# Kernel optimization log

Hardware: AMD Instinct MI355X
Metric: run time of the kernel (lower is better)

Reference implementation:

```python
import jax, jax.numpy as jnp
import numpy as np

B, S, D = 4, 4096, 768

def setup_inputs() -> dict:
    key = jax.random.key(0)
    kx, kq, kk, kv = jax.random.split(key, 4)
    x = jax.random.normal(kx, (B, S, D), dtype=jnp.float32)
    Wq = jax.random.normal(kq, (D, D), dtype=jnp.float32) * (D ** -0.5)
    Wk = jax.random.normal(kk, (D, D), dtype=jnp.float32) * (D ** -0.5)
    Wv = jax.random.normal(kv, (D, D), dtype=jnp.float32) * (D ** -0.5)
    return {"x": x, "Wq": Wq, "Wk": Wk, "Wv": Wv}

def reference(x, Wq, Wk, Wv):
    # q,k,v: [B,S,D]  (Linear with no bias)
    q = x @ Wq
    k = x @ Wk
    v = x @ Wv
    # full N x N causal score matrix, as in the original module
    scores = jnp.einsum('bqd,bkd->bqk', q, k)  # [B,S,S]
    seq = scores.shape[1]
    causal_mask = jnp.triu(jnp.ones((seq, seq), dtype=bool), k=1)  # True above diagonal
    scores = jnp.where(causal_mask[None, :, :], -jnp.inf, scores)
    scale = jnp.asarray(k.shape[-1], scores.dtype) ** 0.5
    weights = jax.nn.softmax(scores / scale, axis=-1)  # [B,S,S]
    # dropout p=0.0 -> identity (deterministic reference)
    context = jnp.einsum('bqk,bkd->bqd', weights, v)  # [B,S,D]
    return context
```

## Files before the change

kernel.cpp:

```cpp
#include <hip/hip_runtime.h>
#include <hip/hip_bf16.h>

typedef __attribute__((ext_vector_type(8))) _Float16 half8_t;
typedef __attribute__((ext_vector_type(4))) _Float16 half4_t;
typedef __attribute__((ext_vector_type(4))) float float4_t;

#define D_DIM 768
#define S_DIM 4096
#define B_DIM 4
#define M_DIM (B_DIM * S_DIM)
#define SD ((size_t)S_DIM * D_DIM)

#define GLOAD_LDS16(g, s)                                      \
  __builtin_amdgcn_global_load_lds(                            \
      (const __attribute__((address_space(1))) void*)(g),      \
      (__attribute__((address_space(3))) void*)(s), 16, 0, 0)

__device__ __forceinline__ float4_t mfma16(half8_t a, half8_t b, float4_t c) {
  return __builtin_amdgcn_mfma_f32_16x16x32_f16(a, b, c, 0, 0, 0);
}

__global__ __launch_bounds__(256) void cvt_x_kernel(const float* __restrict__ in,
                                                    _Float16* __restrict__ out, int n) {
  int i = (blockIdx.x * 256 + threadIdx.x) * 4;
  if (i < n) {
    float4 v = *(const float4*)(in + i);
    half4_t o;
    o.x = (_Float16)v.x; o.y = (_Float16)v.y; o.z = (_Float16)v.z; o.w = (_Float16)v.w;
    *(half4_t*)(out + i) = o;
  }
}

__global__ __launch_bounds__(256) void transpose_w_kernel(const float* __restrict__ W0,
                                                          const float* __restrict__ W1,
                                                          const float* __restrict__ W2,
                                                          _Float16* __restrict__ WT) {
  const float* W = (blockIdx.z == 0) ? W0 : (blockIdx.z == 1) ? W1 : W2;
  _Float16* o = WT + (size_t)blockIdx.z * D_DIM * D_DIM;
  __shared__ _Float16 tile[64][68];
  int k0 = blockIdx.x * 64, n0 = blockIdx.y * 64;
#pragma unroll
  for (int i = 0; i < 16; ++i) {
    int idx = threadIdx.x + i * 256;
    int r = idx >> 6, c = idx & 63;
    tile[r][c] = (_Float16)W[(size_t)(k0 + r) * D_DIM + n0 + c];
  }
  __syncthreads();
#pragma unroll
  for (int i = 0; i < 16; ++i) {
    int idx = threadIdx.x + i * 256;
    int r = idx >> 6, c = idx & 63;
    o[(size_t)(n0 + r) * D_DIM + k0 + c] = tile[c][r];
  }
}

template <bool SWAP>
__device__ __forceinline__ void core256(const _Float16* __restrict__ Ag,
                                        const _Float16* __restrict__ Bg,
                                        int lda, int ldb, int k0, int nt,
                                        char* lds, float4_t (&acc)[8][4]) {
  const int tid = threadIdx.x;
  const int w = tid >> 6, l = tid & 63;
  const int wr = w >> 2, wc = w & 3;
  const int l15 = l & 15, l4 = l >> 4;

  int aSrc[2], bSrc[2], sDst[2];
#pragma unroll
  for (int i = 0; i < 2; ++i) {
    int L = i * 512 + tid;
    int row = L >> 2, u = L & 3;
    int usw = u ^ ((row >> 1) & 3);
    aSrc[i] = row * lda + usw * 8;
    bSrc[i] = row * ldb + usw * 8;
    sDst[i] = (i * 512 + (tid & ~63)) * 16;
  }

#define STG(kt)                                                               \
  do {                                                                        \
    char* slot = lds + ((kt) & 3) * 32768;                                    \
    const _Float16* Asrc = Ag + (size_t)(k0 + (kt)) * 32;                     \
    const _Float16* Bsrc = Bg + (size_t)(k0 + (kt)) * 32;                     \
    _Pragma("unroll") for (int i = 0; i < 2; ++i)                             \
        GLOAD_LDS16(Asrc + aSrc[i], slot + sDst[i]);                          \
    _Pragma("unroll") for (int i = 0; i < 2; ++i)                             \
        GLOAD_LDS16(Bsrc + bSrc[i], slot + 16384 + sDst[i]);                  \
  } while (0)

#pragma unroll
  for (int j = 0; j < 3; ++j)
    if (j < nt) STG(j);

#pragma unroll 1
  for (int kt = 0; kt < nt; ++kt) {
    __builtin_amdgcn_s_barrier();
    if (kt + 3 < nt) STG(kt + 3);
    __builtin_amdgcn_sched_barrier(0);
    if (kt + 3 < nt)
      asm volatile("s_waitcnt vmcnt(12)" ::: "memory");
    else if (kt + 2 < nt)
      asm volatile("s_waitcnt vmcnt(8)" ::: "memory");
    else if (kt + 1 < nt)
      asm volatile("s_waitcnt vmcnt(4)" ::: "memory");
    else
      asm volatile("s_waitcnt vmcnt(0)" ::: "memory");
    __builtin_amdgcn_sched_barrier(0);
    __builtin_amdgcn_s_barrier();
    __builtin_amdgcn_sched_barrier(0);

    const char* As = lds + (kt & 3) * 32768;
    const char* Bs = As + 16384;
    half8_t bf[4];
#pragma unroll
    for (int ni = 0; ni < 4; ++ni) {
      int brow = wc * 64 + ni * 16 + l15;
      bf[ni] = *(const half8_t*)(Bs + brow * 64 + ((l4 ^ ((brow >> 1) & 3)) * 16));
    }
    __builtin_amdgcn_s_setprio(1);
#pragma unroll
    for (int mq = 0; mq < 2; ++mq) {
      half8_t af[4];
#pragma unroll
      for (int mi = 0; mi < 4; ++mi) {
        int arow = wr * 128 + (mq * 4 + mi) * 16 + l15;
        af[mi] = *(const half8_t*)(As + arow * 64 + ((l4 ^ ((arow >> 1) & 3)) * 16));
      }
#pragma unroll
      for (int mi = 0; mi < 4; ++mi)
#pragma unroll
        for (int ni = 0; ni < 4; ++ni) {
          if (SWAP)
            acc[mq * 4 + mi][ni] = mfma16(bf[ni], af[mi], acc[mq * 4 + mi][ni]);
          else
            acc[mq * 4 + mi][ni] = mfma16(af[mi], bf[ni], acc[mq * 4 + mi][ni]);
        }
    }
    __builtin_amdgcn_s_setprio(0);
  }
#undef STG
}

__global__ __launch_bounds__(512, 1) void proj8_kernel(const _Float16* __restrict__ xh,
                                                       const _Float16* __restrict__ WT,
                                                       _Float16* __restrict__ qkv,
                                                       _Float16* __restrict__ vt) {
  __shared__ __align__(16) char lds[131072];
  const int bid = blockIdx.x;
  const int wid = (bid & 7) * 72 + (bid >> 3);
  const int rg2 = wid / 18;
  const int rem = wid % 18;
  const int z = rem / 6;
  const int cb = (rem % 6) >> 1;
  const int rbg = rg2 * 2 + (rem & 1);

  const _Float16* Ag = xh + (size_t)rbg * 256 * D_DIM;
  const _Float16* Bg = WT + (size_t)z * D_DIM * D_DIM + (size_t)cb * 256 * D_DIM;
  float4_t acc[8][4];
#pragma unroll
  for (int a = 0; a < 8; ++a)
#pragma unroll
    for (int b = 0; b < 4; ++b) acc[a][b] = (float4_t){0.f, 0.f, 0.f, 0.f};

  const int tid = threadIdx.x;
  const int w = tid >> 6, l = tid & 63;
  const int wr = w >> 2, wc = w & 3;
  const int l15 = l & 15, l4 = l >> 4;

  if (z < 2) {
    core256<false>(Ag, Bg, D_DIM, D_DIM, 0, 24, lds, acc);
    _Float16* C = qkv + (size_t)z * M_DIM * D_DIM;
#pragma unroll
    for (int mi = 0; mi < 8; ++mi)
#pragma unroll
      for (int ni = 0; ni < 4; ++ni) {
        int col = cb * 256 + wc * 64 + ni * 16 + l15;
#pragma unroll
        for (int j = 0; j < 4; ++j) {
          int row = rbg * 256 + wr * 128 + mi * 16 + l4 * 4 + j;
          C[(size_t)row * D_DIM + col] = (_Float16)acc[mi][ni][j];
        }
      }
  } else {
    core256<true>(Ag, Bg, D_DIM, D_DIM, 0, 24, lds, acc);
#pragma unroll
    for (int mi = 0; mi < 8; ++mi) {
      int scol = rbg * 256 + wr * 128 + mi * 16 + l15;
      int bb = scol >> 12;
      int sl = scol & 4095;
      _Float16* vtb = vt + (size_t)bb * SD;
#pragma unroll
      for (int ni = 0; ni < 4; ++ni) {
#pragma unroll
        for (int j = 0; j < 4; ++j) {
          int drow = cb * 256 + wc * 64 + ni * 16 + l4 * 4 + j;
          vtb[(size_t)drow * S_DIM + sl] = (_Float16)acc[mi][ni][j];
        }
      }
    }
  }
}

__global__ __launch_bounds__(512, 1) void gemm1_8_kernel(const _Float16* __restrict__ Q,
                                                         const _Float16* __restrict__ K,
                                                         _Float16* __restrict__ P,
                                                         float* __restrict__ rp) {
  __shared__ __align__(16) char lds[131072];
  const float SCALE = 0.036084391824351615f;
  const int bid = blockIdx.x;
  const int wid = (bid & 7) * 68 + (bid >> 3);
  const int z = wid / 136;
  const int t = wid % 136;
  int g, base;
  if (t < 10) { g = 0; base = 0; }
  else if (t < 36) { g = 1; base = 10; }
  else if (t < 78) { g = 2; base = 36; }
  else { g = 3; base = 78; }
  int r = t - base;
  int rbg, cb;
  if (r < 16 * g) {
    int cbg = r >> 4, wi = r & 15;
    rbg = 4 * g + (wi >> 2);
    cb = 4 * cbg + (wi & 3);
  } else {
    int r2 = r - 16 * g;
    const int ri[10] = {0, 1, 1, 2, 2, 2, 3, 3, 3, 3};
    const int rj[10] = {0, 0, 1, 0, 1, 2, 0, 1, 2, 3};
    rbg = 4 * g + ri[r2];
    cb = 4 * g + rj[r2];
  }

  const _Float16* Ag = Q + (size_t)z * SD + (size_t)rbg * 256 * D_DIM;
  const _Float16* Bg = K + (size_t)z * SD + (size_t)cb * 256 * D_DIM;
  float4_t acc[8][4];
#pragma unroll
  for (int a = 0; a < 8; ++a)
#pragma unroll
    for (int b = 0; b < 4; ++b) acc[a][b] = (float4_t){0.f, 0.f, 0.f, 0.f};
  core256<false>(Ag, Bg, D_DIM, D_DIM, 0, 24, lds, acc);

  const int tid = threadIdx.x;
  const int w = tid >> 6, l = tid & 63;
  const int wr = w >> 2, wc = w & 3;
  const int l15 = l & 15, l4 = l >> 4;
  _Float16* Pz = P + (size_t)z * S_DIM * S_DIM;
  float* rpz = rp + (size_t)z * S_DIM * 64;
#pragma unroll
  for (int mi = 0; mi < 8; ++mi) {
#pragma unroll
    for (int j = 0; j < 4; ++j) {
      int row = rbg * 256 + wr * 128 + mi * 16 + l4 * 4 + j;
      float rs = 0.f;
#pragma unroll
      for (int ni = 0; ni < 4; ++ni) {
        int col = cb * 256 + wc * 64 + ni * 16 + l15;
        float v = (col <= row) ? __expf(acc[mi][ni][j] * SCALE - 4.0f) : 0.f;
        _Float16 ph = (_Float16)v;
        Pz[(size_t)row * S_DIM + col] = ph;
        rs += (float)ph;
      }
#pragma unroll
      for (int d = 1; d < 16; d <<= 1) rs += __shfl_xor(rs, d);
      if (l15 == 0) rpz[(size_t)row * 64 + cb * 4 + wc] = rs;
    }
  }
}

__global__ __launch_bounds__(256) void rsum_combine_kernel(const float* __restrict__ rp,
                                                           float* __restrict__ rsum) {
  int idx = blockIdx.x * 256 + threadIdx.x;
  int row = idx & 4095;
  int np = ((row >> 8) + 1) * 4;
  const float* p = rp + (size_t)idx * 64;
  float s = 0.f;
  for (int i = 0; i < np; ++i) s += p[i];
  rsum[idx] = s;
}

#define PART_STRIDE ((size_t)4 * 2048 * 768)
__global__ __launch_bounds__(512, 1) void gemm2_8_kernel(const _Float16* __restrict__ P,
                                                         const _Float16* __restrict__ VT,
                                                         float* __restrict__ outp,
                                                         _Float16* __restrict__ part,
                                                         const float* __restrict__ rsum) {
  __shared__ __align__(16) char lds[131072];
  const int bid = blockIdx.x;
  const int wid = (bid & 7) * 26 + (bid >> 3);
  if (wid >= 204) return;
  const int z = wid / 51;
  const int rem = wid % 51;
  const int u = rem / 3;
  const int by = rem % 3;
  int r1, c1, r2 = -1, c2 = 0;
  if (u < 9)        { r1 = 15 - u; c1 = 0; }
  else if (u == 9)  { r1 = 15;     c1 = 1; }
  else if (u < 13)  { r1 = 16 - u; c1 = 0; r2 = u - 10; c2 = 0; }
  else if (u == 13) { r1 = 3;      c1 = 0; r2 = 11;     c2 = 1; }
  else              { r1 = 28 - u; c1 = 1; r2 = u - 6;  c2 = 1; }

  const int tid = threadIdx.x;
  const int w = tid >> 6, l = tid & 63;
  const int wr = w >> 2, wc = w & 3;
  const int l15 = l & 15, l4 = l >> 4;
  const _Float16* Bg = VT + (size_t)z * SD + (size_t)by * 256 * S_DIM;

#pragma unroll 1
  for (int jj = 0; jj < 2; ++jj) {
    const int rbg = jj ? r2 : r1;
    if (rbg < 0) break;
    const int chk = jj ? c2 : c1;
    const int tot = 8 * (rbg + 1);
    const int k0 = chk * 64;
    const int nt = chk ? (tot - 64) : (tot < 64 ? tot : 64);
    const bool split = (tot > 64);
    if (jj) __syncthreads();

    const _Float16* Ag = P + (size_t)z * S_DIM * S_DIM + (size_t)rbg * 256 * S_DIM;
    float4_t acc[8][4];
#pragma unroll
    for (int a = 0; a < 8; ++a)
#pragma unroll
      for (int b = 0; b < 4; ++b) acc[a][b] = (float4_t){0.f, 0.f, 0.f, 0.f};
    core256<false>(Ag, Bg, S_DIM, S_DIM, k0, nt, lds, acc);

#pragma unroll
    for (int mi = 0; mi < 8; ++mi) {
#pragma unroll
      for (int j = 0; j < 4; ++j) {
        int row = rbg * 256 + wr * 128 + mi * 16 + l4 * 4 + j;
        if (!split) {
          float rinv = 1.0f / rsum[(size_t)z * S_DIM + row];
#pragma unroll
          for (int ni = 0; ni < 4; ++ni) {
            int col = by * 256 + wc * 64 + ni * 16 + l15;
            outp[(size_t)z * SD + (size_t)row * D_DIM + col] = acc[mi][ni][j] * rinv;
          }
        } else {
          int lr = row - 2048;
#pragma unroll
          for (int ni = 0; ni < 4; ++ni) {
            int col = by * 256 + wc * 64 + ni * 16 + l15;
            part[(size_t)chk * PART_STRIDE + ((size_t)z * 2048 + lr) * D_DIM + col] =
                (_Float16)acc[mi][ni][j];
          }
        }
      }
    }
  }
}

__global__ __launch_bounds__(256) void g2_combine_kernel(const _Float16* __restrict__ part,
                                                         const float* __restrict__ rsum,
                                                         float* __restrict__ outp) {
  int idx = blockIdx.x * 256 + threadIdx.x;
  int z = idx / 196608;
  int rem = idx - z * 196608;
  int lr = rem / 96, c8 = rem - lr * 96;
  size_t off = ((size_t)z * 2048 + lr) * D_DIM + c8 * 8;
  half8_t p0 = *(const half8_t*)(part + off);
  half8_t p1 = *(const half8_t*)(part + PART_STRIDE + off);
  int row = 2048 + lr;
  float rinv = 1.0f / rsum[(size_t)z * S_DIM + row];
  float* o = outp + (size_t)z * SD + (size_t)row * D_DIM + c8 * 8;
#pragma unroll
  for (int e = 0; e < 8; ++e) o[e] = ((float)p0[e] + (float)p1[e]) * rinv;
}

extern "C" void kernel_launch(void* const* d_in, const int* in_sizes, int n_in,
                              void* d_out, int out_size, void* d_ws, size_t ws_size,
                              hipStream_t stream) {
  const float* x = (const float*)d_in[0];
  const float* Wq = (const float*)d_in[1];
  const float* Wk = (const float*)d_in[2];
  const float* Wv = (const float*)d_in[3];
  float* out = (float*)d_out;
  char* ws = (char*)d_ws;

  const size_t XH_B = (size_t)M_DIM * D_DIM * 2;
  const size_t QKV_B = 3 * XH_B;
  const size_t VT_B = XH_B;
  const size_t WT_B = (size_t)3 * D_DIM * D_DIM * 2;
  const size_t BASE_END = XH_B + QKV_B + VT_B + WT_B;

  _Float16* xh = (_Float16*)ws;
  _Float16* qkv = (_Float16*)(ws + XH_B);
  _Float16* Q = qkv;
  _Float16* K = qkv + (size_t)M_DIM * D_DIM;
  _Float16* vt = (_Float16*)(ws + XH_B + QKV_B);
  _Float16* wt = (_Float16*)(ws + XH_B + QKV_B + VT_B);

  float* rp = (float*)(ws + BASE_END);
  float* rsum = (float*)(ws + BASE_END + (size_t)4194304);
  _Float16* P = (_Float16*)(ws + BASE_END + (size_t)4259840);
  _Float16* part = xh;

  cvt_x_kernel<<<dim3(12288), dim3(256), 0, stream>>>(x, xh, M_DIM * D_DIM);
  transpose_w_kernel<<<dim3(12, 12, 3), dim3(256), 0, stream>>>(Wq, Wk, Wv, wt);
  proj8_kernel<<<dim3(576), dim3(512), 0, stream>>>(xh, wt, qkv, vt);
  gemm1_8_kernel<<<dim3(544), dim3(512), 0, stream>>>(Q, K, P, rp);
  rsum_combine_kernel<<<dim3(64), dim3(256), 0, stream>>>(rp, rsum);
  gemm2_8_kernel<<<dim3(208), dim3(512), 0, stream>>>(P, vt, out, part, rsum);
  g2_combine_kernel<<<dim3(3072), dim3(256), 0, stream>>>(part, rsum, out);
}
```

Measured before the change: 299.7 us.

## Prefetch next k-tile LDS fragments into ping-pong registers in GEMM core

The shared GEMM core now loads the next k-tile's B and first-half A fragments from LDS while the current tile's MFMAs run. It alternates two register sets and unrolls the k-loop by two, and the vmcnt waits are shifted so each stage waits for tile kt+1 instead of kt. The goal is to hide LDS read latency behind matrix-core work. Separately, launch bounds on the three GEMM kernels change from one to two blocks per CU. Each block still uses 128 KB of LDS, so two blocks probably cannot share a CU, and the tighter register budget risks spilling the 128-float accumulator plus the extra fragment registers.

```diff
diff --git a/kernel.cpp b/kernel.cpp
--- a/kernel.cpp
+++ b/kernel.cpp
@@ -73,6 +73,20 @@
     aSrc[i] = row * lda + usw * 8;
     bSrc[i] = row * ldb + usw * 8;
     sDst[i] = (i * 512 + (tid & ~63)) * 16;
+  }
+
+  int bOff[4], a0Off[4], a1Off[4];
+#pragma unroll
+  for (int ni = 0; ni < 4; ++ni) {
+    int brow = wc * 64 + ni * 16 + l15;
+    bOff[ni] = 16384 + brow * 64 + ((l4 ^ ((brow >> 1) & 3)) * 16);
+  }
+#pragma unroll
+  for (int mi = 0; mi < 4; ++mi) {
+    int r0 = wr * 128 + mi * 16 + l15;
+    a0Off[mi] = r0 * 64 + ((l4 ^ ((r0 >> 1) & 3)) * 16);
+    int r1 = wr * 128 + (4 + mi) * 16 + l15;
+    a1Off[mi] = r1 * 64 + ((l4 ^ ((r1 >> 1) & 3)) * 16);
   }
 
 #define STG(kt)                                                               \
@@ -86,60 +100,76 @@
         GLOAD_LDS16(Bsrc + bSrc[i], slot + 16384 + sDst[i]);                  \
   } while (0)
 
-#pragma unroll
-  for (int j = 0; j < 3; ++j)
-    if (j < nt) STG(j);
-
-#pragma unroll 1
-  for (int kt = 0; kt < nt; ++kt) {
+  STG(0);
+  if (nt > 1) STG(1);
+  if (nt > 2) STG(2);
+  if (nt > 2)
+    asm volatile("s_waitcnt vmcnt(4)" ::: "memory");
+  else
+    asm volatile("s_waitcnt vmcnt(0)" ::: "memory");
+  __builtin_amdgcn_s_barrier();
+
+  half8_t bfA[4], a0A[4], bfB[4], a0B[4];
+#pragma unroll
+  for (int i = 0; i < 4; ++i) bfA[i] = *(const half8_t*)(lds + bOff[i]);
+#pragma unroll
+  for (int i = 0; i < 4; ++i) a0A[i] = *(const half8_t*)(lds + a0Off[i]);
+
+  auto phase = [&](int kt, half8_t (&bfC)[4], half8_t (&a0C)[4],
+                   half8_t (&bfN)[4], half8_t (&a0N)[4]) {
     __builtin_amdgcn_s_barrier();
     if (kt + 3 < nt) STG(kt + 3);
     __builtin_amdgcn_sched_barrier(0);
     if (kt + 3 < nt)
-      asm volatile("s_waitcnt vmcnt(12)" ::: "memory");
+      asm volatile("s_waitcnt vmcnt(8)" ::: "memory");
     else if (kt + 2 < nt)
-      asm volatile("s_waitcnt vmcnt(8)" ::: "memory");
-    else if (kt + 1 < nt)
       asm volatile("s_waitcnt vmcnt(4)" ::: "memory");
     else
       asm volatile("s_waitcnt vmcnt(0)" ::: "memory");
     __builtin_amdgcn_sched_barrier(0);
     __builtin_amdgcn_s_barrier();
-    __builtin_amdgcn_sched_barrier(0);
-
-    const char* As = lds + (kt & 3) * 32768;
-    const char* Bs = As + 16384;
-    half8_t bf[4];
-#pragma unroll
-    for (int ni = 0; ni < 4; ++ni) {
-      int brow = wc * 64 + ni * 16 + l15;
-      bf[ni] = *(const half8_t*)(Bs + brow * 64 + ((l4 ^ ((brow >> 1) & 3)) * 16));
+    const char* Sc = lds + (kt & 3) * 32768;
+    half8_t a1[4];
+#pragma unroll
+    for (int i = 0; i < 4; ++i) a1[i] = *(const half8_t*)(Sc + a1Off[i]);
+    if (kt + 1 < nt) {
+      const char* Sn = lds + ((kt + 1) & 3) * 32768;
+#pragma unroll
+      for (int i = 0; i < 4; ++i) bfN[i] = *(const half8_t*)(Sn + bOff[i]);
+#pragma unroll
+      for (int i = 0; i < 4; ++i) a0N[i] = *(const half8_t*)(Sn + a0Off[i]);
     }
     __builtin_amdgcn_s_setprio(1);
 #pragma unroll
-    for (int mq = 0; mq < 2; ++mq) {
-      half8_t af[4];
-#pragma unroll
-      for (int mi = 0; mi < 4; ++mi) {
-        int arow = wr * 128 + (mq * 4 + mi) * 16 + l15;
-        af[mi] = *(const half8_t*)(As + arow * 64 + ((l4 ^ ((arow >> 1) & 3)) * 16));
-      }
-#pragma unroll
-      for (int mi = 0; mi < 4; ++mi)
-#pragma unroll
-        for (int ni = 0; ni < 4; ++ni) {
-          if (SWAP)
-            acc[mq * 4 + mi][ni] = mfma16(bf[ni], af[mi], acc[mq * 4 + mi][ni]);
-          else
-            acc[mq * 4 + mi][ni] = mfma16(af[mi], bf[ni], acc[mq * 4 + mi][ni]);
-        }
-    }
+    for (int mi = 0; mi < 4; ++mi)
+#pragma unroll
+      for (int ni = 0; ni < 4; ++ni) {
+        if (SWAP)
+          acc[mi][ni] = mfma16(bfC[ni], a0C[mi], acc[mi][ni]);
+        else
+          acc[mi][ni] = mfma16(a0C[mi], bfC[ni], acc[mi][ni]);
+      }
+#pragma unroll
+    for (int mi = 0; mi < 4; ++mi)
+#pragma unroll
+      for (int ni = 0; ni < 4; ++ni) {
+        if (SWAP)
+          acc[4 + mi][ni] = mfma16(bfC[ni], a1[mi], acc[4 + mi][ni]);
+        else
+          acc[4 + mi][ni] = mfma16(a1[mi], bfC[ni], acc[4 + mi][ni]);
+      }
     __builtin_amdgcn_s_setprio(0);
+  };
+
+#pragma unroll 1
+  for (int kt = 0; kt < nt; kt += 2) {
+    phase(kt, bfA, a0A, bfB, a0B);
+    phase(kt + 1, bfB, a0B, bfA, a0A);
   }
 #undef STG
 }
 
-__global__ __launch_bounds__(512, 1) void proj8_kernel(const _Float16* __restrict__ xh,
+__global__ __launch_bounds__(512, 2) void proj8_kernel(const _Float16* __restrict__ xh,
                                                        const _Float16* __restrict__ WT,
                                                        _Float16* __restrict__ qkv,
                                                        _Float16* __restrict__ vt) {
@@ -199,7 +229,7 @@
   }
 }
 
-__global__ __launch_bounds__(512, 1) void gemm1_8_kernel(const _Float16* __restrict__ Q,
+__global__ __launch_bounds__(512, 2) void gemm1_8_kernel(const _Float16* __restrict__ Q,
                                                          const _Float16* __restrict__ K,
                                                          _Float16* __restrict__ P,
                                                          float* __restrict__ rp) {
@@ -276,7 +306,7 @@
 }
 
 #define PART_STRIDE ((size_t)4 * 2048 * 768)
-__global__ __launch_bounds__(512, 1) void gemm2_8_kernel(const _Float16* __restrict__ P,
+__global__ __launch_bounds__(512, 2) void gemm2_8_kernel(const _Float16* __restrict__ P,
                                                          const _Float16* __restrict__ VT,
                                                          float* __restrict__ outp,
                                                          _Float16* __restrict__ part,
```

New measurement: 296.1 us. Within noise of the previous version (-1.2%).
